# Performance work log

Measured on AMD Instinct MI355X. Metric: run time of the kernel, lower is better.

Reference implementation:

```python
import jax, jax.numpy as jnp
import numpy as np

N = 4096  # flattened_input_shape


def setup_inputs() -> dict:
    key = jax.random.key(0)
    ks = jax.random.split(key, 5)
    eps = 0.1
    center = jax.random.normal(ks[0], (1, N), dtype=jnp.float32)
    lb0 = center - eps  # initial interval lower bounds [1, N]
    ub0 = center + eps  # initial interval upper bounds [1, N]
    W1 = jax.random.normal(ks[1], (N, N), dtype=jnp.float32) / np.float32(np.sqrt(N))
    b1 = jax.random.normal(ks[2], (1, N), dtype=jnp.float32)
    W2 = jax.random.normal(ks[3], (N, N), dtype=jnp.float32) / np.float32(np.sqrt(N))
    b2 = jax.random.normal(ks[4], (1, N), dtype=jnp.float32)
    raw_alpha = jnp.ones((N,), dtype=jnp.float32)  # nn.Parameter init
    return {"raw_alpha": raw_alpha, "lb0": lb0, "ub0": ub0,
            "W1": W1, "b1": b1, "W2": W2, "b2": b2}


def _pos(x):
    return jnp.where(x > 0, x, jnp.zeros_like(x))


def _neg(x):
    return jnp.where(x < 0, x, jnp.zeros_like(x))


def _forward(raw_alpha, lb0, ub0, W1, b1, W2, b2):
    # ---- previous.backsubstitution(): compose affine2 over affine1 ----
    clslope, clintercept = W2, b2
    cuslope, cuintercept = W2, b2
    clp, cln = _pos(clslope), _neg(clslope)
    cup, cun = _pos(cuslope), _neg(cuslope)
    clintercept = b1 @ clp.T + b1 @ cln.T + clintercept  # [1, N]
    cuintercept = b1 @ cup.T + b1 @ cun.T + cuintercept  # [1, N]
    clslope = clp @ W1 + cln @ W1  # [N, N]
    cuslope = cup @ W1 + cun @ W1  # [N, N]
    # ---- certifier against initial interval bounds ----
    lbounds = lb0 @ _pos(clslope).T + ub0 @ _neg(clslope).T + clintercept  # [1, N]
    ubounds = ub0 @ _pos(cuslope).T + lb0 @ _neg(cuslope).T + cuintercept  # [1, N]
    # ---- DeepPolyReLU transformer ----
    alpha = jax.nn.sigmoid(raw_alpha)  # [N]
    lb = lbounds.reshape(-1)
    ub = ubounds.reshape(-1)
    denom = ub - lb
    # ub/(ub-lb) with NaN (0/0) replaced by 0, grad-safe
    relu_slope = jnp.where(denom == 0, 0.0, ub / jnp.where(denom == 0, 1.0, denom))  # [N]
    relu_intercept = (1.0 - relu_slope)[None, :] * ubounds  # [1, N]
    below = ub <= 0
    above = lb >= 0
    crossing = ~(below | above)
    base = jnp.where(above, 1.0, 0.0)  # [N]
    uslope = jnp.where(crossing, relu_slope, base)
    uintercept = jnp.where(crossing[None, :], relu_intercept, jnp.zeros((1, N), dtype=ubounds.dtype))
    lslope_v1 = jnp.where(crossing, 0.0, base)
    lslope_v2 = jnp.where(crossing, 1.0, base)
    lslope = alpha * lslope_v1 + (1.0 - alpha) * lslope_v2  # [N]
    lintercept = jnp.zeros((1, N), dtype=lbounds.dtype)
    return jnp.diag(lslope), lintercept, jnp.diag(uslope), uintercept


def reference(raw_alpha, lb0, ub0, W1, b1, W2, b2):
    return _forward(raw_alpha, lb0, ub0, W1, b1, W2, b2)
```

## Files before the change

### kernel.cpp

```cpp
#include <hip/hip_runtime.h>
#include <stdint.h>

#define N 4096
#define BM 128
#define BN 128
#define BK 128

#define TILE_BYTES 524288
#define KT_BYTES   16384

#define QSCALE 256.0f
#define INV_QQ (1.0f / 65536.0f)

typedef int v8i __attribute__((ext_vector_type(8)));
typedef float f32x16 __attribute__((ext_vector_type(16)));

union V8 { v8i v; uint4 h[2]; };

__device__ __forceinline__ void gload16(const unsigned char* g, unsigned char* l) {
  __builtin_amdgcn_global_load_lds(
      (const __attribute__((address_space(1))) unsigned int*)g,
      (__attribute__((address_space(3))) unsigned int*)l, 16, 0, 0);
}

__device__ __forceinline__ int pack4_fp8(float a, float b, float c, float d) {
  int r = __builtin_amdgcn_cvt_pk_fp8_f32(a, b, 0, false);
  r = __builtin_amdgcn_cvt_pk_fp8_f32(c, d, r, true);
  return r;
}

__global__ __launch_bounds__(256) void matvec_w1(const float* __restrict__ W1,
                                                 const float* __restrict__ lb0,
                                                 const float* __restrict__ ub0,
                                                 float* __restrict__ tvec,
                                                 float* __restrict__ R_acc) {
  const int k = blockIdx.x;
  const int t = threadIdx.x;
  const float* row = W1 + (size_t)k * N;
  float dot = 0.f;
#pragma unroll
  for (int q = 0; q < 4; ++q) {
    int idx = (q * 256 + t) * 4;
    float4 w = *(const float4*)(row + idx);
    float4 l = *(const float4*)(lb0 + idx);
    float4 u = *(const float4*)(ub0 + idx);
    dot += w.x * 0.5f * (l.x + u.x) + w.y * 0.5f * (l.y + u.y)
         + w.z * 0.5f * (l.z + u.z) + w.w * 0.5f * (l.w + u.w);
  }
  __shared__ float red[256];
  red[t] = dot;
  __syncthreads();
  for (int s = 128; s > 0; s >>= 1) {
    if (t < s) red[t] += red[t + s];
    __syncthreads();
  }
  if (t == 0) {
    tvec[k] = red[0];
    R_acc[k] = 0.f;
  }
}

__global__ __launch_bounds__(256) void convert_w2(const float* __restrict__ W2,
                                                  const float* __restrict__ b1,
                                                  const float* __restrict__ b2,
                                                  const float* __restrict__ tvec,
                                                  unsigned char* __restrict__ W2q,
                                                  float* __restrict__ c,
                                                  float* __restrict__ Sc) {
  const int i = blockIdx.x;
  const int t = threadIdx.x;
  const float* row = W2 + (size_t)i * N;
  float dotb = 0.f, dott = 0.f;
  const int k0 = t * 16;
  alignas(16) int packed[4];
#pragma unroll
  for (int q = 0; q < 4; ++q) {
    int idx = k0 + q * 4;
    float4 w = *(const float4*)(row + idx);
    float4 b = *(const float4*)(b1 + idx);
    float4 tv = *(const float4*)(tvec + idx);
    dotb += w.x * b.x + w.y * b.y + w.z * b.z + w.w * b.w;
    dott += w.x * tv.x + w.y * tv.y + w.z * tv.z + w.w * tv.w;
    packed[q] = pack4_fp8(w.x * QSCALE, w.y * QSCALE, w.z * QSCALE, w.w * QSCALE);
  }
  *(uint4*)(W2q + (size_t)(i >> 7) * TILE_BYTES + (size_t)t * 2048 + (i & 127) * 16) =
      *(const uint4*)packed;

  __shared__ float red[512];
  red[t] = dotb;
  red[t + 256] = dott;
  __syncthreads();
  for (int s = 128; s > 0; s >>= 1) {
    if (t < s) { red[t] += red[t + s]; red[t + 256] += red[t + 256 + s]; }
    __syncthreads();
  }
  if (t == 0) {
    c[i] = red[0] + b2[i];
    Sc[i] = red[256];
  }
}

__global__ __launch_bounds__(256) void transpose_w1(const float* __restrict__ W1,
                                                    unsigned char* __restrict__ W1T) {
  __shared__ float tile[64 * 65];
  const int t = threadIdx.x;
  const int j0 = blockIdx.x * 64, k0 = blockIdx.y * 64;
#pragma unroll
  for (int s = 0; s < 4; ++s) {
    int ck = s * 256 + t;
    int row = ck >> 4;
    int col = (ck & 15) * 4;
    float4 v = *(const float4*)(W1 + (size_t)(k0 + row) * N + j0 + col);
    float* d = &tile[row * 65 + col];
    d[0] = v.x; d[1] = v.y; d[2] = v.z; d[3] = v.w;
  }
  __syncthreads();
  int jl = t >> 2, ch = (t & 3) * 16;
  float f[16];
#pragma unroll
  for (int m = 0; m < 16; ++m) f[m] = tile[(ch + m) * 65 + jl] * QSCALE;
  uint4 o;
  o.x = (unsigned)pack4_fp8(f[0], f[1], f[2], f[3]);
  o.y = (unsigned)pack4_fp8(f[4], f[5], f[6], f[7]);
  o.z = (unsigned)pack4_fp8(f[8], f[9], f[10], f[11]);
  o.w = (unsigned)pack4_fp8(f[12], f[13], f[14], f[15]);
  int j = j0 + jl;
  int kb = k0 + ch;
  *(uint4*)(W1T + (size_t)(j >> 7) * TILE_BYTES + (size_t)(kb >> 7) * KT_BYTES
            + (size_t)((kb >> 4) & 7) * 2048 + (j & 127) * 16) = o;
}

__global__ __launch_bounds__(256, 4) void gemm_absrow(const unsigned char* __restrict__ A,
                                                      const unsigned char* __restrict__ B,
                                                      const float* __restrict__ lb0,
                                                      const float* __restrict__ ub0,
                                                      float* __restrict__ R_acc) {
  __shared__ __align__(16) unsigned char As[BM * BK];
  __shared__ __align__(16) unsigned char Bs[BN * BK];
  const int t = threadIdx.x;
  const int lane = t & 63, w = t >> 6;
  const int wm = (w >> 1) * 64, wn = (w & 1) * 64;
  const int i0 = blockIdx.y * BM, j0 = blockIdx.x * BN;
  const int l31 = lane & 31, half = lane >> 5;

  f32x16 acc[2][2] = {};
  const int sc1 = 0x7F7F7F7F;

  const unsigned char* ga = A + (size_t)blockIdx.y * TILE_BYTES + t * 16;
  const unsigned char* gb = B + (size_t)blockIdx.x * TILE_BYTES + t * 16;

  for (int kt = 0; kt < N / BK; ++kt) {
    __syncthreads();
#pragma unroll
    for (int p = 0; p < 4; ++p) {
      gload16(ga + p * 4096, &As[(p * 256 + t) * 16]);
      gload16(gb + p * 4096, &Bs[(p * 256 + t) * 16]);
    }
    __syncthreads();
#pragma unroll
    for (int h = 0; h < 2; ++h) {
      const int c0 = h * 4 + half * 2;
      V8 af[2], bfr[2];
#pragma unroll
      for (int tm = 0; tm < 2; ++tm) {
        const unsigned char* p = &As[c0 * 2048 + (wm + tm * 32 + l31) * 16];
        af[tm].h[0] = *(const uint4*)p;
        af[tm].h[1] = *(const uint4*)(p + 2048);
      }
#pragma unroll
      for (int tn = 0; tn < 2; ++tn) {
        const unsigned char* p = &Bs[c0 * 2048 + (wn + tn * 32 + l31) * 16];
        bfr[tn].h[0] = *(const uint4*)p;
        bfr[tn].h[1] = *(const uint4*)(p + 2048);
      }
#pragma unroll
      for (int tm = 0; tm < 2; ++tm)
#pragma unroll
        for (int tn = 0; tn < 2; ++tn)
          acc[tm][tn] = __builtin_amdgcn_mfma_scale_f32_32x32x64_f8f6f4(
              af[tm].v, bfr[tn].v, acc[tm][tn],
              0 , 0 ,
              0, sc1, 0, sc1);
    }
    ga += KT_BYTES;
    gb += KT_BYTES;
  }

  float epsv[2];
#pragma unroll
  for (int tn = 0; tn < 2; ++tn) {
    int j = j0 + wn + tn * 32 + l31;
    epsv[tn] = 0.5f * (ub0[j] - lb0[j]);
  }
#pragma unroll
  for (int tm = 0; tm < 2; ++tm) {
#pragma unroll
    for (int r = 0; r < 16; ++r) {
      float s = fabsf(acc[tm][0][r]) * epsv[0] + fabsf(acc[tm][1][r]) * epsv[1];
#pragma unroll
      for (int off = 1; off < 32; off <<= 1)
        s += __shfl_xor(s, off, 64);
      if (l31 == 0) {
        int i = i0 + wm + tm * 32 + (r & 3) + 8 * (r >> 2) + 4 * half;
        atomicAdd(&R_acc[i], s);
      }
    }
  }
}

struct ReluVals { float lslope, uslope, uinter; };

__device__ __forceinline__ ReluVals relu_vals(int i,
                                              const float* __restrict__ cvec,
                                              const float* __restrict__ Sc,
                                              const float* __restrict__ R_acc,
                                              const float* __restrict__ raw_alpha) {
  float mid = Sc[i] + cvec[i];
  float rr = R_acc[i] * INV_QQ;
  float lb = mid - rr;
  float ub = mid + rr;
  float alpha = 1.f / (1.f + expf(-raw_alpha[i]));
  float denom = ub - lb;
  float slope = (denom == 0.f) ? 0.f : ub / denom;
  bool below = ub <= 0.f, above = lb >= 0.f;
  bool crossing = !(below || above);
  float base = above ? 1.f : 0.f;
  ReluVals v;
  v.uslope = crossing ? slope : base;
  v.uinter = crossing ? (1.f - slope) * ub : 0.f;
  float l1 = crossing ? 0.f : base;
  float l2 = crossing ? 1.f : base;
  v.lslope = alpha * l1 + (1.f - alpha) * l2;
  return v;
}

__global__ __launch_bounds__(256) void fill_patch(float4* __restrict__ out, int n4,
                                                  const float* __restrict__ cvec,
                                                  const float* __restrict__ Sc,
                                                  const float* __restrict__ R_acc,
                                                  const float* __restrict__ raw_alpha) {
  const size_t NN = (size_t)N * N;
  const size_t d1_end = NN;
  const size_t d2_beg = NN + N;
  const size_t d2_end = 2 * NN + N;
  int idx = blockIdx.x * 256 + threadIdx.x;
  int stride = gridDim.x * 256;
  for (int i = idx; i < n4; i += stride) {
    size_t e = 4 * (size_t)i;
    float4 v = make_float4(0.f, 0.f, 0.f, 0.f);
    if (e >= d2_end) {
      int b = (int)(e - d2_end);
      v.x = relu_vals(b + 0, cvec, Sc, R_acc, raw_alpha).uinter;
      v.y = relu_vals(b + 1, cvec, Sc, R_acc, raw_alpha).uinter;
      v.z = relu_vals(b + 2, cvec, Sc, R_acc, raw_alpha).uinter;
      v.w = relu_vals(b + 3, cvec, Sc, R_acc, raw_alpha).uinter;
    } else if (e < d1_end) {
      int r = (int)(e >> 12), c = (int)(e & 4095);
      if (r >= c && r < c + 4)
        (&v.x)[r - c] = relu_vals(r, cvec, Sc, R_acc, raw_alpha).lslope;
    } else if (e >= d2_beg) {
      size_t e2 = e - d2_beg;
      int r = (int)(e2 >> 12), c = (int)(e2 & 4095);
      if (r >= c && r < c + 4)
        (&v.x)[r - c] = relu_vals(r, cvec, Sc, R_acc, raw_alpha).uslope;
    }
    out[i] = v;
  }
}

extern "C" void kernel_launch(void* const* d_in, const int* in_sizes, int n_in,
                              void* d_out, int out_size, void* d_ws, size_t ws_size,
                              hipStream_t stream) {
  const float* raw_alpha = (const float*)d_in[0];
  const float* lb0 = (const float*)d_in[1];
  const float* ub0 = (const float*)d_in[2];
  const float* W1 = (const float*)d_in[3];
  const float* b1 = (const float*)d_in[4];
  const float* W2 = (const float*)d_in[5];
  const float* b2 = (const float*)d_in[6];

  float* tvec = (float*)d_ws;
  float* cvec = tvec + N;
  float* Sc = cvec + N;
  float* R_acc = Sc + N;

  unsigned char* W2q = (unsigned char*)d_out;
  unsigned char* W1Tq = W2q + (size_t)N * N;

  matvec_w1<<<N, 256, 0, stream>>>(W1, lb0, ub0, tvec, R_acc);
  convert_w2<<<N, 256, 0, stream>>>(W2, b1, b2, tvec, W2q, cvec, Sc);
  transpose_w1<<<dim3(N / 64, N / 64), 256, 0, stream>>>(W1, W1Tq);
  gemm_absrow<<<dim3(N / BN, N / BM), 256, 0, stream>>>(W2q, W1Tq, lb0, ub0, R_acc);
  int n4 = out_size / 4;
  fill_patch<<<8192, 256, 0, stream>>>((float4*)d_out, n4, cvec, Sc, R_acc, raw_alpha);
}
```

Baseline: 373.7 us.

## Fuse W1 matvec into transpose pass and tile W2 conversion with atomic reductions

Merges the separate W1 mid-point matvec into the W1 transpose/quantize kernel, so W1 is read from global memory once instead of twice. Partial dot products are accumulated in shared-memory atomics, then in global atomics. The W2 conversion kernel is re-tiled into 128x128 blocks that write contiguous fp8 panels and reduce partial row sums with global atomics. The workspace is now zeroed with a memset, and b2 is added later in the fill kernel. This trades an extra full pass over W1 for atomic contention and non-deterministic summation order.

```diff
diff --git a/kernel.cpp b/kernel.cpp
--- a/kernel.cpp
+++ b/kernel.cpp
@@ -29,92 +29,33 @@
   return r;
 }
 
-__global__ __launch_bounds__(256) void matvec_w1(const float* __restrict__ W1,
-                                                 const float* __restrict__ lb0,
-                                                 const float* __restrict__ ub0,
-                                                 float* __restrict__ tvec,
-                                                 float* __restrict__ R_acc) {
-  const int k = blockIdx.x;
-  const int t = threadIdx.x;
-  const float* row = W1 + (size_t)k * N;
-  float dot = 0.f;
-#pragma unroll
-  for (int q = 0; q < 4; ++q) {
-    int idx = (q * 256 + t) * 4;
-    float4 w = *(const float4*)(row + idx);
-    float4 l = *(const float4*)(lb0 + idx);
-    float4 u = *(const float4*)(ub0 + idx);
-    dot += w.x * 0.5f * (l.x + u.x) + w.y * 0.5f * (l.y + u.y)
-         + w.z * 0.5f * (l.z + u.z) + w.w * 0.5f * (l.w + u.w);
-  }
-  __shared__ float red[256];
-  red[t] = dot;
-  __syncthreads();
-  for (int s = 128; s > 0; s >>= 1) {
-    if (t < s) red[t] += red[t + s];
-    __syncthreads();
-  }
-  if (t == 0) {
-    tvec[k] = red[0];
-    R_acc[k] = 0.f;
-  }
-}
-
-__global__ __launch_bounds__(256) void convert_w2(const float* __restrict__ W2,
-                                                  const float* __restrict__ b1,
-                                                  const float* __restrict__ b2,
-                                                  const float* __restrict__ tvec,
-                                                  unsigned char* __restrict__ W2q,
-                                                  float* __restrict__ c,
-                                                  float* __restrict__ Sc) {
-  const int i = blockIdx.x;
-  const int t = threadIdx.x;
-  const float* row = W2 + (size_t)i * N;
-  float dotb = 0.f, dott = 0.f;
-  const int k0 = t * 16;
-  alignas(16) int packed[4];
-#pragma unroll
-  for (int q = 0; q < 4; ++q) {
-    int idx = k0 + q * 4;
-    float4 w = *(const float4*)(row + idx);
-    float4 b = *(const float4*)(b1 + idx);
-    float4 tv = *(const float4*)(tvec + idx);
-    dotb += w.x * b.x + w.y * b.y + w.z * b.z + w.w * b.w;
-    dott += w.x * tv.x + w.y * tv.y + w.z * tv.z + w.w * tv.w;
-    packed[q] = pack4_fp8(w.x * QSCALE, w.y * QSCALE, w.z * QSCALE, w.w * QSCALE);
-  }
-  *(uint4*)(W2q + (size_t)(i >> 7) * TILE_BYTES + (size_t)t * 2048 + (i & 127) * 16) =
-      *(const uint4*)packed;
-
-  __shared__ float red[512];
-  red[t] = dotb;
-  red[t + 256] = dott;
-  __syncthreads();
-  for (int s = 128; s > 0; s >>= 1) {
-    if (t < s) { red[t] += red[t + s]; red[t + 256] += red[t + 256 + s]; }
-    __syncthreads();
-  }
-  if (t == 0) {
-    c[i] = red[0] + b2[i];
-    Sc[i] = red[256];
-  }
-}
-
-__global__ __launch_bounds__(256) void transpose_w1(const float* __restrict__ W1,
-                                                    unsigned char* __restrict__ W1T) {
+__global__ __launch_bounds__(256) void prep_w1(const float* __restrict__ W1,
+                                               const float* __restrict__ lb0,
+                                               const float* __restrict__ ub0,
+                                               unsigned char* __restrict__ W1T,
+                                               float* __restrict__ tvec) {
   __shared__ float tile[64 * 65];
+  __shared__ float tdot[64];
   const int t = threadIdx.x;
   const int j0 = blockIdx.x * 64, k0 = blockIdx.y * 64;
+  if (t < 64) tdot[t] = 0.f;
+  __syncthreads();
 #pragma unroll
   for (int s = 0; s < 4; ++s) {
     int ck = s * 256 + t;
     int row = ck >> 4;
     int col = (ck & 15) * 4;
     float4 v = *(const float4*)(W1 + (size_t)(k0 + row) * N + j0 + col);
+    float4 l = *(const float4*)(lb0 + j0 + col);
+    float4 u = *(const float4*)(ub0 + j0 + col);
+    float part = v.x * 0.5f * (l.x + u.x) + v.y * 0.5f * (l.y + u.y)
+               + v.z * 0.5f * (l.z + u.z) + v.w * 0.5f * (l.w + u.w);
+    atomicAdd(&tdot[row], part);
     float* d = &tile[row * 65 + col];
     d[0] = v.x; d[1] = v.y; d[2] = v.z; d[3] = v.w;
   }
   __syncthreads();
+  if (t < 64) atomicAdd(&tvec[k0 + t], tdot[t]);
   int jl = t >> 2, ch = (t & 3) * 16;
   float f[16];
 #pragma unroll
@@ -128,6 +69,48 @@
   int kb = k0 + ch;
   *(uint4*)(W1T + (size_t)(j >> 7) * TILE_BYTES + (size_t)(kb >> 7) * KT_BYTES
             + (size_t)((kb >> 4) & 7) * 2048 + (j & 127) * 16) = o;
+}
+
+__global__ __launch_bounds__(256) void convert_w2(const float* __restrict__ W2,
+                                                  const float* __restrict__ b1,
+                                                  const float* __restrict__ tvec,
+                                                  unsigned char* __restrict__ W2q,
+                                                  float* __restrict__ cvec,
+                                                  float* __restrict__ Sc) {
+  const int t = threadIdx.x;
+  const int i0 = blockIdx.y * 128;
+  const int k0 = blockIdx.x * 128;
+  const int r = t & 127;
+  const int h = t >> 7;
+  unsigned char* panel = W2q + (size_t)blockIdx.y * TILE_BYTES
+                       + (size_t)blockIdx.x * KT_BYTES;
+  float dotb = 0.f, dott = 0.f;
+#pragma unroll
+  for (int q = 0; q < 4; ++q) {
+    int c = 2 * q + h;
+    const float* p = W2 + (size_t)(i0 + r) * N + k0 + c * 16;
+    alignas(16) int packed[4];
+#pragma unroll
+    for (int m = 0; m < 4; ++m) {
+      float4 w = *(const float4*)(p + m * 4);
+      float4 b = *(const float4*)(b1 + k0 + c * 16 + m * 4);
+      float4 tv = *(const float4*)(tvec + k0 + c * 16 + m * 4);
+      dotb += w.x * b.x + w.y * b.y + w.z * b.z + w.w * b.w;
+      dott += w.x * tv.x + w.y * tv.y + w.z * tv.z + w.w * tv.w;
+      packed[m] = pack4_fp8(w.x * QSCALE, w.y * QSCALE, w.z * QSCALE, w.w * QSCALE);
+    }
+    *(uint4*)(panel + (size_t)c * 2048 + r * 16) = *(const uint4*)packed;
+  }
+  __shared__ float redb[256], redt[256];
+  redb[t] = dotb;
+  redt[t] = dott;
+  __syncthreads();
+  if (t < 128) {
+    float vb = redb[t] + redb[t + 128];
+    float vt = redt[t] + redt[t + 128];
+    atomicAdd(&cvec[i0 + t], vb);
+    atomicAdd(&Sc[i0 + t], vt);
+  }
 }
 
 __global__ __launch_bounds__(256, 4) void gemm_absrow(const unsigned char* __restrict__ A,
@@ -213,9 +196,10 @@
 __device__ __forceinline__ ReluVals relu_vals(int i,
                                               const float* __restrict__ cvec,
                                               const float* __restrict__ Sc,
+                                              const float* __restrict__ b2,
                                               const float* __restrict__ R_acc,
                                               const float* __restrict__ raw_alpha) {
-  float mid = Sc[i] + cvec[i];
+  float mid = Sc[i] + cvec[i] + b2[i];
   float rr = R_acc[i] * INV_QQ;
   float lb = mid - rr;
   float ub = mid + rr;
@@ -237,6 +221,7 @@
 __global__ __launch_bounds__(256) void fill_patch(float4* __restrict__ out, int n4,
                                                   const float* __restrict__ cvec,
                                                   const float* __restrict__ Sc,
+                                                  const float* __restrict__ b2,
                                                   const float* __restrict__ R_acc,
                                                   const float* __restrict__ raw_alpha) {
   const size_t NN = (size_t)N * N;
@@ -250,19 +235,19 @@
     float4 v = make_float4(0.f, 0.f, 0.f, 0.f);
     if (e >= d2_end) {
       int b = (int)(e - d2_end);
-      v.x = relu_vals(b + 0, cvec, Sc, R_acc, raw_alpha).uinter;
-      v.y = relu_vals(b + 1, cvec, Sc, R_acc, raw_alpha).uinter;
-      v.z = relu_vals(b + 2, cvec, Sc, R_acc, raw_alpha).uinter;
-      v.w = relu_vals(b + 3, cvec, Sc, R_acc, raw_alpha).uinter;
+      v.x = relu_vals(b + 0, cvec, Sc, b2, R_acc, raw_alpha).uinter;
+      v.y = relu_vals(b + 1, cvec, Sc, b2, R_acc, raw_alpha).uinter;
+      v.z = relu_vals(b + 2, cvec, Sc, b2, R_acc, raw_alpha).uinter;
+      v.w = relu_vals(b + 3, cvec, Sc, b2, R_acc, raw_alpha).uinter;
     } else if (e < d1_end) {
       int r = (int)(e >> 12), c = (int)(e & 4095);
       if (r >= c && r < c + 4)
-        (&v.x)[r - c] = relu_vals(r, cvec, Sc, R_acc, raw_alpha).lslope;
+        (&v.x)[r - c] = relu_vals(r, cvec, Sc, b2, R_acc, raw_alpha).lslope;
     } else if (e >= d2_beg) {
       size_t e2 = e - d2_beg;
       int r = (int)(e2 >> 12), c = (int)(e2 & 4095);
       if (r >= c && r < c + 4)
-        (&v.x)[r - c] = relu_vals(r, cvec, Sc, R_acc, raw_alpha).uslope;
+        (&v.x)[r - c] = relu_vals(r, cvec, Sc, b2, R_acc, raw_alpha).uslope;
     }
     out[i] = v;
   }
@@ -287,10 +272,10 @@
   unsigned char* W2q = (unsigned char*)d_out;
   unsigned char* W1Tq = W2q + (size_t)N * N;
 
-  matvec_w1<<<N, 256, 0, stream>>>(W1, lb0, ub0, tvec, R_acc);
-  convert_w2<<<N, 256, 0, stream>>>(W2, b1, b2, tvec, W2q, cvec, Sc);
-  transpose_w1<<<dim3(N / 64, N / 64), 256, 0, stream>>>(W1, W1Tq);
+  (void)hipMemsetAsync(d_ws, 0, 4 * N * sizeof(float), stream);
+  prep_w1<<<dim3(N / 64, N / 64), 256, 0, stream>>>(W1, lb0, ub0, W1Tq, tvec);
+  convert_w2<<<dim3(N / 128, N / 128), 256, 0, stream>>>(W2, b1, tvec, W2q, cvec, Sc);
   gemm_absrow<<<dim3(N / BN, N / BM), 256, 0, stream>>>(W2q, W1Tq, lb0, ub0, R_acc);
   int n4 = out_size / 4;
-  fill_patch<<<8192, 256, 0, stream>>>((float4*)d_out, n4, cvec, Sc, R_acc, raw_alpha);
-}
+  fill_patch<<<8192, 256, 0, stream>>>((float4*)d_out, n4, cvec, Sc, b2, R_acc, raw_alpha);
+}
```

After: 353.0 us. 5.5% less time.
